# Optimization experiments

Hardware: AMD Instinct MI355X
Metric: run time of the kernel (lower is better)

The kernel has to match this reference:

```python
import jax, jax.numpy as jnp
import numpy as np

N_ENT = 100000   # entities / graph nodes
N_REL = 500      # relations (table has 2*N_REL rows: fwd+inv)
H = 256          # hidden dim
E = 320000       # edges


def setup_inputs() -> dict:
    key = jax.random.key(0)
    ks = jax.random.split(key, 9)
    std = (2.0 / (H + H)) ** 0.5  # xavier_normal for (H,H)
    return {
        "ent_emb": jax.random.normal(ks[0], (N_ENT, H), dtype=jnp.float32),
        "rel_emb": jax.random.normal(ks[1], (2 * N_REL, H), dtype=jnp.float32),
        "w_edge": jax.random.normal(ks[2], (H, H), dtype=jnp.float32) * std,
        "w_node": jax.random.normal(ks[3], (H, H), dtype=jnp.float32) * std,
        "w_comp": jax.random.normal(ks[4], (H, H), dtype=jnp.float32) * std,
        "rel_w": jax.random.normal(ks[5], (H, H), dtype=jnp.float32) * std,
        "src": jax.random.randint(ks[6], (E,), 0, N_ENT, dtype=jnp.int32),
        "dst": jax.random.randint(ks[7], (E,), 0, N_ENT, dtype=jnp.int32),
        "rel_id": jax.random.randint(ks[8], (E,), 0, 2 * N_REL, dtype=jnp.int32),
        "node_id": jnp.arange(N_ENT, dtype=jnp.int32),
    }


def _edge_softmax(score, dst, n):
    # per-destination-node softmax over incoming edges (DGL edge_softmax)
    m = jax.ops.segment_max(score, dst, num_segments=n)
    ex = jnp.exp(score - m[dst])
    s = jax.ops.segment_sum(ex, dst, num_segments=n)
    return ex / s[dst]


def reference(ent_emb, rel_emb, w_edge, w_node, w_comp, rel_w,
              src, dst, rel_id, node_id):
    n = ent_emb.shape[0]
    h = ent_emb[node_id]          # [N, H] (node_id maps node -> entity row)
    hs = h[src]                   # [E, H] source node features
    hd = h[dst]                   # [E, H] destination node features
    e = rel_emb[rel_id]           # [E, H] edge (relation) features

    # EdgeLayer: e . h_dst -> edge_softmax -> scatter-sum(e * a) -> W -> tanh
    a_e = _edge_softmax(jnp.sum(e * hd, axis=-1), dst, n)
    edge_out = jnp.tanh(
        jax.ops.segment_sum(e * a_e[:, None], dst, num_segments=n) @ w_edge)

    # NodeLayer: h_src . h_dst -> edge_softmax -> scatter-sum(h_src * a)
    a_n = _edge_softmax(jnp.sum(hs * hd, axis=-1), dst, n)
    node_out = jnp.tanh(
        jax.ops.segment_sum(hs * a_n[:, None], dst, num_segments=n) @ w_node)

    # CompLayer (mul): comp = h_src * e ; comp . h_dst -> softmax -> scatter-sum
    comp = hs * e
    a_c = _edge_softmax(jnp.sum(comp * hd, axis=-1), dst, n)
    comp_out = jnp.tanh(
        jax.ops.segment_sum(comp * a_c[:, None], dst, num_segments=n) @ w_comp)

    out_ent = ent_emb + edge_out + node_out + comp_out
    out_rel = rel_emb @ rel_w
    return (out_ent, out_rel)
```

## Files before the change

### kernel.cpp

```cpp
#include <hip/hip_runtime.h>
#include <hip/hip_bf16.h>

#define N_ENT  100000
#define N_REL2 1000
#define H      256
#define E_EDGES 320000
#define REL_ROWS_PAD 1024

typedef unsigned short u16;
typedef short bf16x8 __attribute__((ext_vector_type(8)));
typedef float floatx4 __attribute__((ext_vector_type(4)));

__device__ __forceinline__ u16 f2bf(float f) {
    unsigned x = __float_as_uint(f);
    unsigned r = (x + 0x7fffu + ((x >> 16) & 1u)) >> 16;
    return (u16)r;
}

__device__ __forceinline__ ushort4 pack4(float4 v, float s) {
    return make_ushort4(f2bf(v.x * s), f2bf(v.y * s), f2bf(v.z * s), f2bf(v.w * s));
}

__device__ __forceinline__ float fast_tanh(float x) {
    float e = __expf(2.0f * x);
    return 1.0f - 2.0f * __builtin_amdgcn_rcpf(e + 1.0f);
}

__device__ __forceinline__ void async16(u16* lds, const u16* g) {
    __builtin_amdgcn_global_load_lds(
        (const __attribute__((address_space(1))) void*)g,
        (__attribute__((address_space(3))) void*)lds, 16, 0, 0);
}


__global__ void hist_kernel(const int* __restrict__ dst, int* __restrict__ counts) {
    int i = blockIdx.x * blockDim.x + threadIdx.x;
    if (i < E_EDGES) atomicAdd(&counts[dst[i]], 1);
}

__global__ void scan1_kernel(const int* __restrict__ counts, int* __restrict__ offsets,
                             int* __restrict__ bsum) {
    __shared__ int buf[1024];
    int t = threadIdx.x, i = blockIdx.x * 1024 + t;
    int v = (i < N_ENT) ? counts[i] : 0;
    int acc = v;
    buf[t] = acc;
    __syncthreads();
    for (int off = 1; off < 1024; off <<= 1) {
        int u = (t >= off) ? buf[t - off] : 0;
        __syncthreads();
        acc += u;
        buf[t] = acc;
        __syncthreads();
    }
    if (i < N_ENT) offsets[i] = acc - v;
    if (t == 1023) bsum[blockIdx.x] = acc;
}

__global__ void scan2_kernel(int* __restrict__ bsum, int* __restrict__ offsets) {
    __shared__ int s[128];
    int t = threadIdx.x;
    s[t] = (t < 98) ? bsum[t] : 0;
    __syncthreads();
    if (t == 0) {
        int run = 0;
        for (int b = 0; b < 98; ++b) { int x = s[b]; s[b] = run; run += x; }
        offsets[N_ENT] = run;
    }
    __syncthreads();
    if (t < 98) bsum[t] = s[t];
}

__global__ void scan3_kernel(int* __restrict__ offsets, const int* __restrict__ bsum) {
    int i = blockIdx.x * 1024 + threadIdx.x;
    if (i < N_ENT && blockIdx.x > 0) offsets[i] += bsum[blockIdx.x];
}

__global__ void place_kernel(const int* __restrict__ dst, const int* __restrict__ src,
                             const int* __restrict__ rel_id, const int* __restrict__ node_id,
                             const int* __restrict__ offsets,
                             int* __restrict__ counts, int2* __restrict__ meta) {
    int i = blockIdx.x * blockDim.x + threadIdx.x;
    if (i < E_EDGES) {
        int d = dst[i];
        int old = atomicSub(&counts[d], 1);
        meta[offsets[d] + old - 1] = make_int2(node_id[src[i]], rel_id[i]);
    }
}

__global__ void swz_kernel(const float* __restrict__ w0, const float* __restrict__ w1,
                           const float* __restrict__ w2, const float* __restrict__ w3,
                           u16* __restrict__ dstp) {
    int t = blockIdx.x * blockDim.x + threadIdx.x;
    if (t >= 4 * H * H) return;
    int mat = t >> 16;
    int r = t & 65535;
    int j = r & 7, lane = (r >> 3) & 63, kstep = (r >> 9) & 7, ntile = r >> 12;
    int k = kstep * 32 + (lane >> 4) * 8 + j;
    int n = ntile * 16 + (lane & 15);
    const float* W = (mat == 0) ? w0 : (mat == 1) ? w1 : (mat == 2) ? w2 : w3;
    dstp[t] = f2bf(W[k * H + n]);
}

__global__ void relbf_kernel(const float* __restrict__ rel, u16* __restrict__ out) {
    int t = blockIdx.x * blockDim.x + threadIdx.x;
    if (t >= REL_ROWS_PAD * H) return;
    int row = t >> 8, kk = t & 255;
    int k = kk ^ ((row & 7) << 3);
    float v = (row < N_REL2) ? rel[row * H + k] : 0.f;
    out[t] = f2bf(v);
}

__global__ __launch_bounds__(256) void scatter_kernel(
    const float* __restrict__ ent, const float* __restrict__ rel,
    const int2* __restrict__ meta, const int* __restrict__ node_id,
    const int* __restrict__ offsets,
    u16* __restrict__ agg_e, u16* __restrict__ agg_n, u16* __restrict__ agg_c) {
    int lane = threadIdx.x & 63;
    int wv = __builtin_amdgcn_readfirstlane(threadIdx.x >> 6);
    int d = blockIdx.x * 4 + wv;
    if (d >= N_ENT) return;
    int nid = node_id[d];
    int p0 = offsets[d], p1 = offsets[d + 1];
    float4 hd = ((const float4*)(ent + (size_t)nid * H))[lane];
    float me = -INFINITY, mn = -INFINITY, mc = -INFINITY;
    float le = 0.f, ln = 0.f, lc = 0.f;
    float4 ae = make_float4(0, 0, 0, 0), an = make_float4(0, 0, 0, 0), ac = make_float4(0, 0, 0, 0);

    for (int pc = p0; pc < p1; pc += 4) {
        int cnt = p1 - pc; if (cnt > 4) cnt = 4;
        int2 md[4];
#pragma unroll
        for (int j = 0; j < 4; ++j) if (j < cnt) md[j] = meta[pc + j];
        float4 ev[4], sv[4];
#pragma unroll
        for (int j = 0; j < 4; ++j) if (j < cnt) {
            ev[j] = ((const float4*)(rel + (size_t)md[j].y * H))[lane];
            sv[j] = ((const float4*)(ent + (size_t)md[j].x * H))[lane];
        }
#pragma unroll
        for (int j = 0; j < 4; ++j) if (j < cnt) {
            float4 e4 = ev[j], s4 = sv[j];
            float4 c4 = make_float4(e4.x * s4.x, e4.y * s4.y, e4.z * s4.z, e4.w * s4.w);
            float de = e4.x * hd.x + e4.y * hd.y + e4.z * hd.z + e4.w * hd.w;
            float dn = s4.x * hd.x + s4.y * hd.y + s4.z * hd.z + s4.w * hd.w;
            float dc = c4.x * hd.x + c4.y * hd.y + c4.z * hd.z + c4.w * hd.w;
#pragma unroll
            for (int o = 32; o > 0; o >>= 1) {
                de += __shfl_xor(de, o);
                dn += __shfl_xor(dn, o);
                dc += __shfl_xor(dc, o);
            }
            { float nm = fmaxf(me, de); float s = __expf(me - nm); float pr = __expf(de - nm);
              le = le * s + pr;
              ae.x = ae.x * s + pr * e4.x; ae.y = ae.y * s + pr * e4.y;
              ae.z = ae.z * s + pr * e4.z; ae.w = ae.w * s + pr * e4.w; me = nm; }
            { float nm = fmaxf(mn, dn); float s = __expf(mn - nm); float pr = __expf(dn - nm);
              ln = ln * s + pr;
              an.x = an.x * s + pr * s4.x; an.y = an.y * s + pr * s4.y;
              an.z = an.z * s + pr * s4.z; an.w = an.w * s + pr * s4.w; mn = nm; }
            { float nm = fmaxf(mc, dc); float s = __expf(mc - nm); float pr = __expf(dc - nm);
              lc = lc * s + pr;
              ac.x = ac.x * s + pr * c4.x; ac.y = ac.y * s + pr * c4.y;
              ac.z = ac.z * s + pr * c4.z; ac.w = ac.w * s + pr * c4.w; mc = nm; }
        }
    }
    float ie = (le > 0.f) ? 1.0f / le : 0.f;
    float in_ = (ln > 0.f) ? 1.0f / ln : 0.f;
    float ic = (lc > 0.f) ? 1.0f / lc : 0.f;
    size_t rowb = (size_t)d * (H * 2);
    int boff = (lane * 8) ^ ((d & 7) << 4);
    *(ushort4*)((char*)agg_e + rowb + boff) = pack4(ae, ie);
    *(ushort4*)((char*)agg_n + rowb + boff) = pack4(an, in_);
    *(ushort4*)((char*)agg_c + rowb + boff) = pack4(ac, ic);
}

__global__ __launch_bounds__(256, 2) void gemm_kernel(
    const u16* __restrict__ A0, const u16* __restrict__ A1, const u16* __restrict__ A2,
    const u16* __restrict__ W0, const u16* __restrict__ W1, const u16* __restrict__ W2,
    const float* __restrict__ base, float* __restrict__ out,
    int n_real, int n_layers, int do_tanh) {
    __shared__ u16 lA[2][16384];
    int tid = threadIdx.x;
    int lane = tid & 63;
    int wv = tid >> 6;
    int m = lane & 15;
    int quad = lane >> 4;
    int r0 = blockIdx.x * 64;
    const u16* As[3] = { A0, A1, A2 };
    const u16* Ws[3] = { W0, W1, W2 };

    float outacc[4][4][4];
#pragma unroll
    for (int rt = 0; rt < 4; ++rt)
#pragma unroll
        for (int ct = 0; ct < 4; ++ct) {
            int grow = r0 + rt * 16 + quad * 4;
            int gcol = wv * 64 + ct * 16 + m;
#pragma unroll
            for (int r = 0; r < 4; ++r) {
                float v = 0.f;
                if (base != nullptr && (grow + r) < n_real) v = base[(size_t)(grow + r) * H + gcol];
                outacc[rt][ct][r] = v;
            }
        }

    {
        const u16* gsrc = As[0] + (size_t)blockIdx.x * 64 * H;
#pragma unroll
        for (int rnd = 0; rnd < 8; ++rnd) {
            int off8 = (rnd * 256 + tid) * 8;
            async16(&lA[0][off8], gsrc + off8);
        }
    }

    int mrow = m * 512;
    int swz = (m & 7) << 4;

    for (int l = 0; l < n_layers; ++l) {
        __syncthreads();
        if (l + 1 < n_layers) {
            const u16* gsrc = As[l + 1] + (size_t)blockIdx.x * 64 * H;
            u16* dstb = lA[(l + 1) & 1];
#pragma unroll
            for (int rnd = 0; rnd < 8; ++rnd) {
                int off8 = (rnd * 256 + tid) * 8;
                async16(&dstb[off8], gsrc + off8);
            }
        }
        const char* lbc = (const char*)lA[l & 1];
        const u16* Wl = Ws[l];

        floatx4 lacc[4][4];
#pragma unroll
        for (int rt = 0; rt < 4; ++rt)
#pragma unroll
            for (int ct = 0; ct < 4; ++ct)
#pragma unroll
                for (int r = 0; r < 4; ++r) lacc[rt][ct][r] = 0.f;

#pragma unroll
        for (int ks = 0; ks < 8; ++ks) {
            bf16x8 af[4], bfr[4];
#pragma unroll
            for (int rt = 0; rt < 4; ++rt)
                af[rt] = *(const bf16x8*)(lbc + rt * 8192 + mrow + ((ks * 64 + quad * 16) ^ swz));
#pragma unroll
            for (int ct = 0; ct < 4; ++ct)
                bfr[ct] = *(const bf16x8*)(Wl + (((size_t)(wv * 4 + ct) * 8 + ks) * 64 + lane) * 8);
#pragma unroll
            for (int rt = 0; rt < 4; ++rt)
#pragma unroll
                for (int ct = 0; ct < 4; ++ct)
                    lacc[rt][ct] = __builtin_amdgcn_mfma_f32_16x16x32_bf16(
                        af[rt], bfr[ct], lacc[rt][ct], 0, 0, 0);
        }

#pragma unroll
        for (int rt = 0; rt < 4; ++rt)
#pragma unroll
            for (int ct = 0; ct < 4; ++ct)
#pragma unroll
                for (int r = 0; r < 4; ++r) {
                    float v = lacc[rt][ct][r];
                    outacc[rt][ct][r] += do_tanh ? fast_tanh(v) : v;
                }
    }

#pragma unroll
    for (int rt = 0; rt < 4; ++rt)
#pragma unroll
        for (int ct = 0; ct < 4; ++ct) {
            int grow = r0 + rt * 16 + quad * 4;
            int gcol = wv * 64 + ct * 16 + m;
#pragma unroll
            for (int r = 0; r < 4; ++r)
                if ((grow + r) < n_real) out[(size_t)(grow + r) * H + gcol] = outacc[rt][ct][r];
        }
}


extern "C" void kernel_launch(void* const* d_in, const int* in_sizes, int n_in,
                              void* d_out, int out_size, void* d_ws, size_t ws_size,
                              hipStream_t stream) {
    (void)in_sizes; (void)n_in; (void)out_size; (void)ws_size;
    const float* ent    = (const float*)d_in[0];
    const float* rel    = (const float*)d_in[1];
    const float* w_edge = (const float*)d_in[2];
    const float* w_node = (const float*)d_in[3];
    const float* w_comp = (const float*)d_in[4];
    const float* rel_w  = (const float*)d_in[5];
    const int* src      = (const int*)d_in[6];
    const int* dst      = (const int*)d_in[7];
    const int* rel_id   = (const int*)d_in[8];
    const int* node_id  = (const int*)d_in[9];

    char* wsb = (char*)d_ws;
    size_t o = 0;
    auto alloc = [&](size_t bytes) -> char* {
        char* p = wsb + o;
        o = (o + bytes + 255) & ~(size_t)255;
        return p;
    };
    int* counts  = (int*)alloc((size_t)N_ENT * 4);
    int* offsets = (int*)alloc((size_t)(N_ENT + 1) * 4);
    int* bsum    = (int*)alloc(128 * 4);
    int2* meta   = (int2*)alloc((size_t)E_EDGES * 8);
    u16* agg_e   = (u16*)alloc((size_t)N_ENT * H * 2);
    u16* agg_n   = (u16*)alloc((size_t)N_ENT * H * 2);
    u16* agg_c   = (u16*)alloc((size_t)N_ENT * H * 2);
    u16* wswz    = (u16*)alloc((size_t)4 * H * H * 2);
    u16* relbf   = (u16*)alloc((size_t)REL_ROWS_PAD * H * 2);
    (void)alloc(65536);

    float* out_ent = (float*)d_out;
    float* out_rel = out_ent + (size_t)N_ENT * H;

    hipMemsetAsync(counts, 0, (size_t)N_ENT * 4, stream);
    hist_kernel<<<(E_EDGES + 255) / 256, 256, 0, stream>>>(dst, counts);
    scan1_kernel<<<98, 1024, 0, stream>>>(counts, offsets, bsum);
    scan2_kernel<<<1, 128, 0, stream>>>(bsum, offsets);
    scan3_kernel<<<98, 1024, 0, stream>>>(offsets, bsum);
    place_kernel<<<(E_EDGES + 255) / 256, 256, 0, stream>>>(dst, src, rel_id, node_id,
                                                            offsets, counts, meta);
    swz_kernel<<<(4 * H * H + 255) / 256, 256, 0, stream>>>(w_edge, w_node, w_comp, rel_w, wswz);
    relbf_kernel<<<(REL_ROWS_PAD * H + 255) / 256, 256, 0, stream>>>(rel, relbf);
    scatter_kernel<<<N_ENT / 4, 256, 0, stream>>>(ent, rel, meta, node_id, offsets,
                                                  agg_e, agg_n, agg_c);
    gemm_kernel<<<(N_ENT + 63) / 64, 256, 0, stream>>>(agg_e, agg_n, agg_c,
                                                       wswz, wswz + H * H, wswz + 2 * H * H,
                                                       ent, out_ent, N_ENT, 3, 1);
    gemm_kernel<<<(N_REL2 + 63) / 64, 256, 0, stream>>>(relbf, relbf, relbf,
                                                        wswz + 3 * H * H, wswz + 3 * H * H, wswz + 3 * H * H,
                                                        nullptr, out_rel, N_REL2, 1, 0);
}
```

Before: 498.3 us.

## Sort destination nodes by in-degree before scatter to balance wavefront work

Adds a counting sort of destination nodes by in-degree (histogram, scan, placement) and makes the scatter kernel look up its node through this order. Each 4-wave block then handles nodes with similar edge counts, which is meant to cut intra-block load imbalance and tail divergence. It costs three extra small kernel launches plus atomics, and destination writes and hd reads become less sequential.

```diff
diff --git a/kernel.cpp b/kernel.cpp
--- a/kernel.cpp
+++ b/kernel.cpp
@@ -6,6 +6,7 @@
 #define H      256
 #define E_EDGES 320000
 #define REL_ROWS_PAD 1024
+#define DEG_BINS 64
 
 typedef unsigned short u16;
 typedef short bf16x8 __attribute__((ext_vector_type(8)));
@@ -76,6 +77,32 @@
     if (i < N_ENT && blockIdx.x > 0) offsets[i] += bsum[blockIdx.x];
 }
 
+
+__global__ void deghist_kernel(const int* __restrict__ counts, int* __restrict__ dbin) {
+    int i = blockIdx.x * blockDim.x + threadIdx.x;
+    if (i < N_ENT) {
+        int b = counts[i]; if (b > DEG_BINS - 1) b = DEG_BINS - 1;
+        atomicAdd(&dbin[b], 1);
+    }
+}
+
+__global__ void degscan_kernel(const int* __restrict__ dbin, int* __restrict__ doff) {
+    if (threadIdx.x == 0) {
+        int run = 0;
+        for (int b = 0; b < DEG_BINS; ++b) { doff[b] = run; run += dbin[b]; }
+    }
+}
+
+__global__ void degplace_kernel(const int* __restrict__ counts, int* __restrict__ doff,
+                                int* __restrict__ dorder) {
+    int i = blockIdx.x * blockDim.x + threadIdx.x;
+    if (i < N_ENT) {
+        int b = counts[i]; if (b > DEG_BINS - 1) b = DEG_BINS - 1;
+        int pos = atomicAdd(&doff[b], 1);
+        dorder[pos] = i;
+    }
+}
+
 __global__ void place_kernel(const int* __restrict__ dst, const int* __restrict__ src,
                              const int* __restrict__ rel_id, const int* __restrict__ node_id,
                              const int* __restrict__ offsets,
@@ -114,12 +141,13 @@
 __global__ __launch_bounds__(256) void scatter_kernel(
     const float* __restrict__ ent, const float* __restrict__ rel,
     const int2* __restrict__ meta, const int* __restrict__ node_id,
-    const int* __restrict__ offsets,
+    const int* __restrict__ offsets, const int* __restrict__ dorder,
     u16* __restrict__ agg_e, u16* __restrict__ agg_n, u16* __restrict__ agg_c) {
     int lane = threadIdx.x & 63;
     int wv = __builtin_amdgcn_readfirstlane(threadIdx.x >> 6);
-    int d = blockIdx.x * 4 + wv;
-    if (d >= N_ENT) return;
+    int w = blockIdx.x * 4 + wv;
+    if (w >= N_ENT) return;
+    int d = dorder[w];
     int nid = node_id[d];
     int p0 = offsets[d], p1 = offsets[d + 1];
     float4 hd = ((const float4*)(ent + (size_t)nid * H))[lane];
@@ -306,6 +334,9 @@
     int* offsets = (int*)alloc((size_t)(N_ENT + 1) * 4);
     int* bsum    = (int*)alloc(128 * 4);
     int2* meta   = (int2*)alloc((size_t)E_EDGES * 8);
+    int* dbin    = (int*)alloc(DEG_BINS * 4);
+    int* doff    = (int*)alloc(DEG_BINS * 4);
+    int* dorder  = (int*)alloc((size_t)N_ENT * 4);
     u16* agg_e   = (u16*)alloc((size_t)N_ENT * H * 2);
     u16* agg_n   = (u16*)alloc((size_t)N_ENT * H * 2);
     u16* agg_c   = (u16*)alloc((size_t)N_ENT * H * 2);
@@ -317,15 +348,19 @@
     float* out_rel = out_ent + (size_t)N_ENT * H;
 
     hipMemsetAsync(counts, 0, (size_t)N_ENT * 4, stream);
+    hipMemsetAsync(dbin, 0, DEG_BINS * 4, stream);
     hist_kernel<<<(E_EDGES + 255) / 256, 256, 0, stream>>>(dst, counts);
     scan1_kernel<<<98, 1024, 0, stream>>>(counts, offsets, bsum);
     scan2_kernel<<<1, 128, 0, stream>>>(bsum, offsets);
     scan3_kernel<<<98, 1024, 0, stream>>>(offsets, bsum);
+    deghist_kernel<<<(N_ENT + 255) / 256, 256, 0, stream>>>(counts, dbin);
+    degscan_kernel<<<1, 64, 0, stream>>>(dbin, doff);
+    degplace_kernel<<<(N_ENT + 255) / 256, 256, 0, stream>>>(counts, doff, dorder);
     place_kernel<<<(E_EDGES + 255) / 256, 256, 0, stream>>>(dst, src, rel_id, node_id,
                                                             offsets, counts, meta);
     swz_kernel<<<(4 * H * H + 255) / 256, 256, 0, stream>>>(w_edge, w_node, w_comp, rel_w, wswz);
     relbf_kernel<<<(REL_ROWS_PAD * H + 255) / 256, 256, 0, stream>>>(rel, relbf);
-    scatter_kernel<<<N_ENT / 4, 256, 0, stream>>>(ent, rel, meta, node_id, offsets,
+    scatter_kernel<<<N_ENT / 4, 256, 0, stream>>>(ent, rel, meta, node_id, offsets, dorder,
                                                   agg_e, agg_n, agg_c);
     gemm_kernel<<<(N_ENT + 63) / 64, 256, 0, stream>>>(agg_e, agg_n, agg_c,
                                                        wswz, wswz + H * H, wswz + 2 * H * H,
```

Measured after the change: 1.351 ms. 2.71x slower.
